# Optimization experiments

Measured on AMD Instinct MI355X. Metric: run time of the kernel, lower is better.

The kernel has to match this reference:

```python
import jax, jax.numpy as jnp
import numpy as np

N = 100000      # nodes
E = 1600000     # edges (avg degree 16)
F_IN = 256      # num_features
H2 = 128        # nhid * 2 (layer 1 width)
H = 64          # nhid (layer 2 width)
C = 10          # num_classes


def setup_inputs() -> dict:
    key = jax.random.key(0)
    ks = jax.random.split(key, 8)
    x = jax.random.normal(ks[0], (N, F_IN), dtype=jnp.float32)
    edge_index = jax.random.randint(ks[1], (2, E), 0, N, dtype=jnp.int64)
    W1 = jax.random.normal(ks[2], (F_IN, H2), dtype=jnp.float32) / np.float32(np.sqrt(F_IN))
    b1 = jnp.zeros((H2,), jnp.float32)
    W2 = jax.random.normal(ks[3], (H2, H), dtype=jnp.float32) / np.float32(np.sqrt(H2))
    b2 = jnp.zeros((H,), jnp.float32)
    Wl = jax.random.normal(ks[4], (H, C), dtype=jnp.float32) / np.float32(np.sqrt(H))
    bl = jnp.zeros((C,), jnp.float32)
    return {"x": x, "edge_index": edge_index, "W1": W1, "b1": b1,
            "W2": W2, "b2": b2, "Wl": Wl, "bl": bl}


def reference(x, edge_index, W1, b1, W2, b2, Wl, bl):
    # --- GCN normalization with self-loops (PyG GCNConv default) ---
    loops = jnp.arange(N, dtype=edge_index.dtype)
    src = jnp.concatenate([edge_index[0], loops])  # message sources
    dst = jnp.concatenate([edge_index[1], loops])  # message targets
    deg = jax.ops.segment_sum(jnp.ones(src.shape[0], x.dtype), dst, num_segments=N)
    dinv = jnp.where(deg > 0, jax.lax.rsqrt(deg), 0.0)
    norm = dinv[src] * dinv[dst]                   # [E+N]

    def gcn_conv(h, W, b):
        m = h @ W                                  # transform first (out_channels small)
        agg = jax.ops.segment_sum(m[src] * norm[:, None], dst, num_segments=N)
        return agg + b

    h = jax.nn.relu(gcn_conv(x, W1, b1))           # [N, H2]
    h = jax.nn.relu(gcn_conv(h, W2, b2))           # [N, H]
    logits = h @ Wl + bl                            # [N, C]
    return jax.nn.log_softmax(logits, axis=-1)
```

## Files before the change

kernel.cpp:

```cpp
#include <hip/hip_runtime.h>


typedef unsigned short ushort_t;
typedef unsigned int uint_t;
typedef __attribute__((ext_vector_type(8))) short short8;
typedef __attribute__((ext_vector_type(4))) float floatx4;

static __device__ __forceinline__ ushort_t f2bf(float f) {
    union { float f; uint_t u; } c; c.f = f;
    return (ushort_t)((c.u + 0x8000u) >> 16);
}
static __device__ __forceinline__ float bf2f(ushort_t h) {
    union { uint_t u; float f; } c; c.u = ((uint_t)h) << 16;
    return c.f;
}
static __device__ __forceinline__ float2 up2(uint_t p) {
    union { uint_t u; float f; } lo, hi;
    lo.u = p << 16; hi.u = p & 0xffff0000u;
    return make_float2(lo.f, hi.f);
}
static __device__ __forceinline__ uint_t pk2bf(float a, float b) {
    return ((uint_t)f2bf(b) << 16) | (uint_t)f2bf(a);
}
static __device__ __forceinline__ void ld_lds16(void* lds, const void* g) {
    __builtin_amdgcn_global_load_lds(
        (const __attribute__((address_space(1))) unsigned int*)g,
        (__attribute__((address_space(3))) unsigned int*)lds, 16, 0, 0);
}

#define NBMAX 800
#define ECAP  4096

__global__ __launch_bounds__(256) void hist_kernel(
    const int* __restrict__ dst, int* __restrict__ histG, int E, int NB) {
    __shared__ int h[NBMAX];
    for (int i = threadIdx.x; i < NB; i += 256) h[i] = 0;
    __syncthreads();
    int i8 = (blockIdx.x * 256 + threadIdx.x) * 8;
    if (i8 + 7 < E) {
        int4 d0 = *(const int4*)(dst + i8);
        int4 d1 = *(const int4*)(dst + i8 + 4);
        atomicAdd(&h[d0.x >> 7], 1);
        atomicAdd(&h[d0.y >> 7], 1);
        atomicAdd(&h[d0.z >> 7], 1);
        atomicAdd(&h[d0.w >> 7], 1);
        atomicAdd(&h[d1.x >> 7], 1);
        atomicAdd(&h[d1.y >> 7], 1);
        atomicAdd(&h[d1.z >> 7], 1);
        atomicAdd(&h[d1.w >> 7], 1);
    } else {
        for (int e = i8; e < E; e++) atomicAdd(&h[dst[e] >> 7], 1);
    }
    __syncthreads();
    int* out = histG + (size_t)blockIdx.x * NB;
    for (int i = threadIdx.x; i < NB; i += 256) out[i] = h[i];
}

__global__ __launch_bounds__(256) void scan_bucket(
    int* __restrict__ histG, int* __restrict__ totG, int GB, int NB) {
    __shared__ int s[256];
    const int b = blockIdx.x;
    const int t = threadIdx.x;
    int running = 0;
    int nch = (GB + 255) / 256;
    for (int c = 0; c < nch; c++) {
        int j = c * 256 + t;
        int v = (j < GB) ? histG[(size_t)j * NB + b] : 0;
        s[t] = v;
        __syncthreads();
        for (int off = 1; off < 256; off <<= 1) {
            int tmp = (t >= off) ? s[t - off] : 0;
            __syncthreads();
            s[t] += tmp;
            __syncthreads();
        }
        if (j < GB) histG[(size_t)j * NB + b] = s[t] - v + running;
        int ctot = s[255];
        __syncthreads();
        running += ctot;
    }
    if (t == 0) totG[b] = running;
}

__global__ void scan_tot(const int* __restrict__ totG, int* __restrict__ bbase,
                         int NB) {
    __shared__ int s[256];
    const int t = threadIdx.x;
    int running = 0;
    int nch = (NB + 255) / 256;
    for (int c = 0; c < nch; c++) {
        int j = c * 256 + t;
        int v = (j < NB) ? totG[j] : 0;
        s[t] = v;
        __syncthreads();
        for (int off = 1; off < 256; off <<= 1) {
            int tmp = (t >= off) ? s[t - off] : 0;
            __syncthreads();
            s[t] += tmp;
            __syncthreads();
        }
        if (j < NB) bbase[j] = s[t] - v + running;
        int ctot = s[255];
        __syncthreads();
        running += ctot;
    }
    if (t == 0) bbase[NB] = running;
}

__global__ __launch_bounds__(256) void scatter_kernel(
    const int* __restrict__ src, const int* __restrict__ dst,
    const int* __restrict__ histG, const int* __restrict__ bbase,
    int* __restrict__ packed, int E, int NB) {
    __shared__ int lbase[NBMAX];
    const int* row = histG + (size_t)blockIdx.x * NB;
    for (int i = threadIdx.x; i < NB; i += 256)
        lbase[i] = bbase[i] + row[i];
    __syncthreads();
    int i8 = (blockIdx.x * 256 + threadIdx.x) * 8;
    if (i8 + 7 < E) {
        int4 s0 = *(const int4*)(src + i8);
        int4 s1 = *(const int4*)(src + i8 + 4);
        int4 d0 = *(const int4*)(dst + i8);
        int4 d1 = *(const int4*)(dst + i8 + 4);
        int p;
        p = atomicAdd(&lbase[d0.x >> 7], 1); packed[p] = s0.x | ((d0.x & 127) << 17);
        p = atomicAdd(&lbase[d0.y >> 7], 1); packed[p] = s0.y | ((d0.y & 127) << 17);
        p = atomicAdd(&lbase[d0.z >> 7], 1); packed[p] = s0.z | ((d0.z & 127) << 17);
        p = atomicAdd(&lbase[d0.w >> 7], 1); packed[p] = s0.w | ((d0.w & 127) << 17);
        p = atomicAdd(&lbase[d1.x >> 7], 1); packed[p] = s1.x | ((d1.x & 127) << 17);
        p = atomicAdd(&lbase[d1.y >> 7], 1); packed[p] = s1.y | ((d1.y & 127) << 17);
        p = atomicAdd(&lbase[d1.z >> 7], 1); packed[p] = s1.z | ((d1.z & 127) << 17);
        p = atomicAdd(&lbase[d1.w >> 7], 1); packed[p] = s1.w | ((d1.w & 127) << 17);
    } else {
        for (int e = i8; e < E; e++) {
            int d = dst[e];
            int p = atomicAdd(&lbase[d >> 7], 1);
            packed[p] = src[e] | ((d & 127) << 17);
        }
    }
}

__global__ __launch_bounds__(256) void bucket_csr(
    const int* __restrict__ packed, const int* __restrict__ bbase,
    int* __restrict__ rowptr, int* __restrict__ csr,
    float* __restrict__ dinv, int N, int NB) {
    __shared__ int ebuf[ECAP];
    __shared__ int cnt[128];
    __shared__ int pl[128];
    __shared__ int s[256];
    const int b = blockIdx.x;
    const int t = threadIdx.x;
    const int lo = bbase[b];
    const int hi = bbase[b + 1];
    int m = hi - lo;
    if (m > ECAP) m = ECAP;
    for (int i = t; i < m; i += 256) ebuf[i] = packed[lo + i];
    if (t < 128) cnt[t] = 0;
    __syncthreads();
    for (int i = t; i < m; i += 256) atomicAdd(&cnt[ebuf[i] >> 17], 1);
    __syncthreads();
    const int node0 = b << 7;
    int c = (t < 128) ? cnt[t] : 0;
    if (t < 128 && node0 + t < N)
        dinv[node0 + t] = rsqrtf((float)(c + 1));
    s[t] = c;
    __syncthreads();
    for (int off = 1; off < 256; off <<= 1) {
        int tmp = (t >= off) ? s[t - off] : 0;
        __syncthreads();
        s[t] += tmp;
        __syncthreads();
    }
    int excl = s[t] - c;
    if (t < 128) {
        pl[t] = excl;
        if (node0 + t <= N) rowptr[node0 + t] = lo + excl;
    }
    __syncthreads();
    for (int i = t; i < m; i += 256) {
        int e = ebuf[i];
        int p = atomicAdd(&pl[e >> 17], 1);
        csr[lo + p] = e & 0x1FFFF;
    }
}

__global__ void wcvt2_kernel(const float* __restrict__ W1, const float* __restrict__ W2,
                             ushort_t* __restrict__ W1t, ushort_t* __restrict__ W2t) {
    int i = blockIdx.x * 256 + threadIdx.x;
    if (i < 256 * 128) {
        int k = i / 128, n = i % 128;
        W1t[n * 256 + k] = f2bf(W1[i]);
    }
    int j = i - 256 * 128;
    if (j >= 0 && j < 128 * 64) {
        int k = j / 64, n = j % 64;
        W2t[n * 128 + k] = f2bf(W2[j]);
    }
}

__global__ __launch_bounds__(256) void gemm1_mfma(
    const float* __restrict__ A, const ushort_t* __restrict__ Bt,
    const float* __restrict__ dinv, ushort_t* __restrict__ out, int M) {
    __shared__ ushort_t As[2][128 * 40];
    __shared__ ushort_t Bs[2][128 * 32];
    const int tid = threadIdx.x;
    const int l = tid & 63;
    const int wave = tid >> 6;
    const int wm = wave >> 1, wn = wave & 1;
    const int lrow = l & 15, hh = l >> 4;
    const int m0 = blockIdx.x * 128;

    const int srow = tid >> 1, sh = tid & 1;
    int grow = m0 + srow; if (grow >= M) grow = M - 1;
    const float* gA = A + (size_t)grow * 256 + sh * 16;
    const int wslot = srow * 40 + sh * 16;

    int aslot[4], bslot[4];
    #pragma unroll
    for (int mt = 0; mt < 4; mt++) {
        int r = wm * 64 + mt * 16 + lrow;
        aslot[mt] = r * 40 + hh * 8;
    }
    #pragma unroll
    for (int nt = 0; nt < 4; nt++) {
        int nc = wn * 64 + nt * 16 + lrow;
        bslot[nt] = (nc * 4 + (hh ^ ((nc >> 2) & 3))) * 8;
    }

    floatx4 acc[4][4];
    #pragma unroll
    for (int mt = 0; mt < 4; mt++)
        #pragma unroll
        for (int nt = 0; nt < 4; nt++)
            acc[mt][nt] = (floatx4){0.f, 0.f, 0.f, 0.f};

    float4 ar[4];
    auto loadA = [&](int k0) {
        #pragma unroll
        for (int i = 0; i < 4; i++)
            ar[i] = *(const float4*)(gA + k0 + i * 4);
    };
    auto writeA = [&](int buf) {
        uint4 q0, q1;
        q0.x = pk2bf(ar[0].x, ar[0].y); q0.y = pk2bf(ar[0].z, ar[0].w);
        q0.z = pk2bf(ar[1].x, ar[1].y); q0.w = pk2bf(ar[1].z, ar[1].w);
        q1.x = pk2bf(ar[2].x, ar[2].y); q1.y = pk2bf(ar[2].z, ar[2].w);
        q1.z = pk2bf(ar[3].x, ar[3].y); q1.w = pk2bf(ar[3].z, ar[3].w);
        *(uint4*)&As[buf][wslot] = q0;
        *(uint4*)&As[buf][wslot + 8] = q1;
    };
    auto stageB = [&](int buf, int k0) {
        #pragma unroll
        for (int i = 0; i < 2; i++) {
            int s = i * 256 + tid;
            int nn = s >> 2, cp = s & 3;
            int cg = cp ^ ((nn >> 2) & 3);
            ld_lds16(&Bs[buf][s * 8], Bt + (size_t)nn * 256 + k0 + cg * 8);
        }
    };

    loadA(0);
    stageB(0, 0);
    writeA(0);
    __syncthreads();

    int buf = 0;
    for (int kk = 0; kk < 8; kk++) {
        if (kk < 7) {
            loadA((kk + 1) * 32);
            stageB(buf ^ 1, (kk + 1) * 32);
        }
        short8 afr[4], bfr[4];
        #pragma unroll
        for (int mt = 0; mt < 4; mt++)
            afr[mt] = *(const short8*)&As[buf][aslot[mt]];
        #pragma unroll
        for (int nt = 0; nt < 4; nt++)
            bfr[nt] = *(const short8*)&Bs[buf][bslot[nt]];
        #pragma unroll
        for (int mt = 0; mt < 4; mt++)
            #pragma unroll
            for (int nt = 0; nt < 4; nt++)
                acc[mt][nt] = __builtin_amdgcn_mfma_f32_16x16x32_bf16(
                    afr[mt], bfr[nt], acc[mt][nt], 0, 0, 0);
        if (kk < 7) writeA(buf ^ 1);
        __syncthreads();
        buf ^= 1;
    }

    const int r0 = hh * 4;
    #pragma unroll
    for (int mt = 0; mt < 4; mt++) {
        int mbase = m0 + wm * 64 + mt * 16 + r0;
        float4 dv = *(const float4*)&dinv[mbase];
        float d[4] = {dv.x, dv.y, dv.z, dv.w};
        #pragma unroll
        for (int i = 0; i < 4; i++) {
            int m = mbase + i;
            if (m < M) {
                #pragma unroll
                for (int nt = 0; nt < 4; nt++)
                    out[(size_t)m * 128 + wn * 64 + nt * 16 + lrow] =
                        f2bf(acc[mt][nt][i] * d[i]);
            }
        }
    }
}

__global__ __launch_bounds__(256) void gemm2_mfma(
    const ushort_t* __restrict__ A, const ushort_t* __restrict__ Bt,
    const float* __restrict__ dinv, ushort_t* __restrict__ out, int M) {
    __shared__ ushort_t As[2][128 * 32];
    __shared__ ushort_t Bs[2][64 * 32];
    const int tid = threadIdx.x;
    const int l = tid & 63;
    const int wave = tid >> 6;
    const int wm = wave >> 1, wn = wave & 1;
    const int lrow = l & 15, hh = l >> 4;
    const int m0 = blockIdx.x * 128;

    int aslot[4], bslot[2];
    #pragma unroll
    for (int mt = 0; mt < 4; mt++) {
        int r = wm * 64 + mt * 16 + lrow;
        aslot[mt] = (r * 4 + (hh ^ ((r >> 2) & 3))) * 8;
    }
    #pragma unroll
    for (int nt = 0; nt < 2; nt++) {
        int nc = wn * 32 + nt * 16 + lrow;
        bslot[nt] = (nc * 4 + (hh ^ ((nc >> 2) & 3))) * 8;
    }

    floatx4 acc[4][2];
    #pragma unroll
    for (int mt = 0; mt < 4; mt++)
        #pragma unroll
        for (int nt = 0; nt < 2; nt++)
            acc[mt][nt] = (floatx4){0.f, 0.f, 0.f, 0.f};

    auto stage = [&](int buf, int k0) {
        #pragma unroll
        for (int i = 0; i < 2; i++) {
            int s = i * 256 + tid;
            int r = s >> 2, cp = s & 3;
            int cg = cp ^ ((r >> 2) & 3);
            int row = m0 + r; if (row >= M) row = M - 1;
            ld_lds16(&As[buf][s * 8], A + (size_t)row * 128 + k0 + cg * 8);
        }
        {
            int s = tid;
            int nn = s >> 2, cp = s & 3;
            int cg = cp ^ ((nn >> 2) & 3);
            ld_lds16(&Bs[buf][s * 8], Bt + (size_t)nn * 128 + k0 + cg * 8);
        }
    };

    stage(0, 0);
    __syncthreads();
    int buf = 0;
    for (int kk = 0; kk < 4; kk++) {
        if (kk < 3) stage(buf ^ 1, (kk + 1) * 32);
        short8 afr[4], bfr[2];
        #pragma unroll
        for (int mt = 0; mt < 4; mt++)
            afr[mt] = *(const short8*)&As[buf][aslot[mt]];
        #pragma unroll
        for (int nt = 0; nt < 2; nt++)
            bfr[nt] = *(const short8*)&Bs[buf][bslot[nt]];
        #pragma unroll
        for (int mt = 0; mt < 4; mt++)
            #pragma unroll
            for (int nt = 0; nt < 2; nt++)
                acc[mt][nt] = __builtin_amdgcn_mfma_f32_16x16x32_bf16(
                    afr[mt], bfr[nt], acc[mt][nt], 0, 0, 0);
        __syncthreads();
        buf ^= 1;
    }

    const int r0 = hh * 4;
    #pragma unroll
    for (int mt = 0; mt < 4; mt++) {
        int mbase = m0 + wm * 64 + mt * 16 + r0;
        float4 dv = *(const float4*)&dinv[mbase];
        float d[4] = {dv.x, dv.y, dv.z, dv.w};
        #pragma unroll
        for (int i = 0; i < 4; i++) {
            int m = mbase + i;
            if (m < M) {
                #pragma unroll
                for (int nt = 0; nt < 2; nt++)
                    out[(size_t)m * 64 + wn * 32 + nt * 16 + lrow] =
                        f2bf(acc[mt][nt][i] * d[i]);
            }
        }
    }
}

__global__ __launch_bounds__(256) void spmm_relu128(
    const ushort_t* __restrict__ Mm, const int* __restrict__ rowptr,
    const int* __restrict__ csr, const float* __restrict__ dinv,
    const float* __restrict__ bias, ushort_t* __restrict__ out, int n, int doff) {
    int v = (blockIdx.x * 256 + threadIdx.x) >> 6;
    int lane = threadIdx.x & 63;
    if (v >= n) return;
    int jb = rowptr[v];
    int cntn = rowptr[v + 1] - jb;
    const char* Mb = (const char*)Mm;
    const int slot = lane >> 4;
    const int q = lane & 15;
    const uint_t qb = (uint_t)q * 16;

    float2 a0 = {0.f, 0.f}, a1 = a0, a2 = a0, a3 = a0;
    if (slot == 0) {
        uint4 s = *(const uint4*)(Mb + ((size_t)v << 8) + qb);
        a0 = up2(s.x); a1 = up2(s.y); a2 = up2(s.z); a3 = up2(s.w);
    }

    for (int base = 0; base < cntn; base += 64) {
        int m = cntn - base; if (m > 64) m = 64;
        int roff = (base + lane < cntn) ? (csr[jb + base + lane] << 8) : doff;
        int m4 = (m + 3) & ~3;
        int jj = 0;
        for (; jj + 16 <= m4; jj += 16) {
            uint_t o[4];
            #pragma unroll
            for (int t = 0; t < 4; t++)
                o[t] = (uint_t)__shfl(roff, jj + 4 * t + slot) + qb;
            uint4 p[4];
            #pragma unroll
            for (int t = 0; t < 4; t++) p[t] = *(const uint4*)(Mb + o[t]);
            #pragma unroll
            for (int t = 0; t < 4; t++) {
                float2 f;
                f = up2(p[t].x); a0.x += f.x; a0.y += f.y;
                f = up2(p[t].y); a1.x += f.x; a1.y += f.y;
                f = up2(p[t].z); a2.x += f.x; a2.y += f.y;
                f = up2(p[t].w); a3.x += f.x; a3.y += f.y;
            }
        }
        for (; jj < m4; jj += 4) {
            uint_t o = (uint_t)__shfl(roff, jj + slot) + qb;
            uint4 p = *(const uint4*)(Mb + o);
            float2 f;
            f = up2(p.x); a0.x += f.x; a0.y += f.y;
            f = up2(p.y); a1.x += f.x; a1.y += f.y;
            f = up2(p.z); a2.x += f.x; a2.y += f.y;
            f = up2(p.w); a3.x += f.x; a3.y += f.y;
        }
    }
    float r[8] = {a0.x, a0.y, a1.x, a1.y, a2.x, a2.y, a3.x, a3.y};
    #pragma unroll
    for (int i = 0; i < 8; i++) r[i] += __shfl_xor(r[i], 16);
    #pragma unroll
    for (int i = 0; i < 8; i++) r[i] += __shfl_xor(r[i], 32);
    if (slot == 0) {
        float d = dinv[v];
        float4 bv0 = *(const float4*)&bias[q * 8];
        float4 bv1 = *(const float4*)&bias[q * 8 + 4];
        float o0 = fmaxf(d * r[0] + bv0.x, 0.f);
        float o1 = fmaxf(d * r[1] + bv0.y, 0.f);
        float o2 = fmaxf(d * r[2] + bv0.z, 0.f);
        float o3 = fmaxf(d * r[3] + bv0.w, 0.f);
        float o4 = fmaxf(d * r[4] + bv1.x, 0.f);
        float o5 = fmaxf(d * r[5] + bv1.y, 0.f);
        float o6 = fmaxf(d * r[6] + bv1.z, 0.f);
        float o7 = fmaxf(d * r[7] + bv1.w, 0.f);
        uint4 pk;
        pk.x = pk2bf(o0, o1); pk.y = pk2bf(o2, o3);
        pk.z = pk2bf(o4, o5); pk.w = pk2bf(o6, o7);
        *(uint4*)(out + (size_t)v * 128 + q * 8) = pk;
    }
}

__global__ __launch_bounds__(256) void spmm_relu64(
    const ushort_t* __restrict__ Mm, const int* __restrict__ rowptr,
    const int* __restrict__ csr, const float* __restrict__ dinv,
    const float* __restrict__ bias, ushort_t* __restrict__ out, int n, int doff) {
    int v = (blockIdx.x * 256 + threadIdx.x) >> 6;
    int lane = threadIdx.x & 63;
    if (v >= n) return;
    int jb = rowptr[v];
    int cntn = rowptr[v + 1] - jb;
    const char* Mb = (const char*)Mm;
    const int slot = lane >> 3;
    const int q = lane & 7;
    const uint_t qb = (uint_t)q * 16;

    float2 a0 = {0.f, 0.f}, a1 = a0, a2 = a0, a3 = a0;
    if (slot == 0) {
        uint4 s = *(const uint4*)(Mb + ((size_t)v << 7) + qb);
        a0 = up2(s.x); a1 = up2(s.y); a2 = up2(s.z); a3 = up2(s.w);
    }

    for (int base = 0; base < cntn; base += 64) {
        int m = cntn - base; if (m > 64) m = 64;
        int roff = (base + lane < cntn) ? (csr[jb + base + lane] << 7) : doff;
        int m8 = (m + 7) & ~7;
        int jj = 0;
        for (; jj + 16 <= m8; jj += 16) {
            uint_t o[2];
            #pragma unroll
            for (int t = 0; t < 2; t++)
                o[t] = (uint_t)__shfl(roff, jj + 8 * t + slot) + qb;
            uint4 p[2];
            #pragma unroll
            for (int t = 0; t < 2; t++) p[t] = *(const uint4*)(Mb + o[t]);
            #pragma unroll
            for (int t = 0; t < 2; t++) {
                float2 f;
                f = up2(p[t].x); a0.x += f.x; a0.y += f.y;
                f = up2(p[t].y); a1.x += f.x; a1.y += f.y;
                f = up2(p[t].z); a2.x += f.x; a2.y += f.y;
                f = up2(p[t].w); a3.x += f.x; a3.y += f.y;
            }
        }
        for (; jj < m8; jj += 8) {
            uint_t o = (uint_t)__shfl(roff, jj + slot) + qb;
            uint4 p = *(const uint4*)(Mb + o);
            float2 f;
            f = up2(p.x); a0.x += f.x; a0.y += f.y;
            f = up2(p.y); a1.x += f.x; a1.y += f.y;
            f = up2(p.z); a2.x += f.x; a2.y += f.y;
            f = up2(p.w); a3.x += f.x; a3.y += f.y;
        }
    }
    float r[8] = {a0.x, a0.y, a1.x, a1.y, a2.x, a2.y, a3.x, a3.y};
    #pragma unroll
    for (int i = 0; i < 8; i++) r[i] += __shfl_xor(r[i], 8);
    #pragma unroll
    for (int i = 0; i < 8; i++) r[i] += __shfl_xor(r[i], 16);
    #pragma unroll
    for (int i = 0; i < 8; i++) r[i] += __shfl_xor(r[i], 32);
    if (slot == 0) {
        float d = dinv[v];
        float4 bv0 = *(const float4*)&bias[q * 8];
        float4 bv1 = *(const float4*)&bias[q * 8 + 4];
        float o0 = fmaxf(d * r[0] + bv0.x, 0.f);
        float o1 = fmaxf(d * r[1] + bv0.y, 0.f);
        float o2 = fmaxf(d * r[2] + bv0.z, 0.f);
        float o3 = fmaxf(d * r[3] + bv0.w, 0.f);
        float o4 = fmaxf(d * r[4] + bv1.x, 0.f);
        float o5 = fmaxf(d * r[5] + bv1.y, 0.f);
        float o6 = fmaxf(d * r[6] + bv1.z, 0.f);
        float o7 = fmaxf(d * r[7] + bv1.w, 0.f);
        uint4 pk;
        pk.x = pk2bf(o0, o1); pk.y = pk2bf(o2, o3);
        pk.z = pk2bf(o4, o5); pk.w = pk2bf(o6, o7);
        *(uint4*)(out + (size_t)v * 64 + q * 8) = pk;
    }
}

__global__ __launch_bounds__(256) void head_kernel(
    const ushort_t* __restrict__ h2, const float* __restrict__ Wl,
    const float* __restrict__ bl, float* __restrict__ out, int n) {
    __shared__ float Ws[64 * 10];
    __shared__ float bs[10];
    for (int i = threadIdx.x; i < 640; i += 256) Ws[i] = Wl[i];
    if (threadIdx.x < 10) bs[threadIdx.x] = bl[threadIdx.x];
    __syncthreads();
    int v = blockIdx.x * 256 + threadIdx.x;
    if (v >= n) return;
    float acc[10];
    #pragma unroll
    for (int c = 0; c < 10; c++) acc[c] = bs[c];
    const ushort_t* hrow = &h2[(size_t)v * 64];
    #pragma unroll
    for (int k0 = 0; k0 < 64; k0 += 8) {
        short8 hv = *(const short8*)&hrow[k0];
        #pragma unroll
        for (int kk = 0; kk < 8; kk++) {
            float hf = bf2f((ushort_t)hv[kk]);
            #pragma unroll
            for (int c = 0; c < 10; c++)
                acc[c] += hf * Ws[(k0 + kk) * 10 + c];
        }
    }
    float m = acc[0];
    #pragma unroll
    for (int c = 1; c < 10; c++) m = fmaxf(m, acc[c]);
    float s = 0.f;
    #pragma unroll
    for (int c = 0; c < 10; c++) s += expf(acc[c] - m);
    float lse = logf(s);
    #pragma unroll
    for (int c = 0; c < 10; c++) out[(size_t)v * 10 + c] = acc[c] - m - lse;
}

extern "C" void kernel_launch(void* const* d_in, const int* in_sizes, int n_in,
                              void* d_out, int out_size, void* d_ws, size_t ws_size,
                              hipStream_t stream) {
    const float* x   = (const float*)d_in[0];
    const int*   ei  = (const int*)d_in[1];
    const float* W1  = (const float*)d_in[2];
    const float* b1  = (const float*)d_in[3];
    const float* W2  = (const float*)d_in[4];
    const float* b2  = (const float*)d_in[5];
    const float* Wl  = (const float*)d_in[6];
    const float* bl  = (const float*)d_in[7];
    float*       out = (float*)d_out;

    const int N = in_sizes[0] / 256;
    const int E = in_sizes[1] / 2;
    const int* srcI = ei;
    const int* dstI = ei + E;

    const int NB = (N + 127) >> 7;
    const int GB = (E + 2047) / 2048;

    char* ws = (char*)d_ws;
    size_t off = 0;
    auto alloc = [&](size_t bytes) -> void* {
        void* p = ws + off;
        off = (off + bytes + 255) & ~(size_t)255;
        return p;
    };
    int*      histG  = (int*)alloc((size_t)GB * NB * 4);
    int*      totG   = (int*)alloc((size_t)NB * 4);
    int*      bbase  = (int*)alloc((size_t)(NB + 1) * 4);
    int*      packed = (int*)alloc((size_t)E * 4);
    int*      rowptr = (int*)alloc((size_t)(N + 1) * 4);
    float*    dinv   = (float*)alloc((size_t)(N + 128) * 4);
    int*      csr    = (int*)alloc((size_t)E * 4);
    ushort_t* W1t    = (ushort_t*)alloc((size_t)128 * 256 * 2);
    ushort_t* W2t    = (ushort_t*)alloc((size_t)64 * 128 * 2);
    ushort_t* bufA   = (ushort_t*)alloc((size_t)(N + 2) * 128 * 2);
    ushort_t* bufB   = (ushort_t*)alloc((size_t)N * 128 * 2);

    hist_kernel<<<GB, 256, 0, stream>>>(dstI, histG, E, NB);
    scan_bucket<<<NB, 256, 0, stream>>>(histG, totG, GB, NB);
    scan_tot<<<1, 256, 0, stream>>>(totG, bbase, NB);
    scatter_kernel<<<GB, 256, 0, stream>>>(srcI, dstI, histG, bbase, packed, E, NB);
    bucket_csr<<<NB, 256, 0, stream>>>(packed, bbase, rowptr, csr, dinv, N, NB);

    wcvt2_kernel<<<(256 * 128 + 128 * 64 + 255) / 256, 256, 0, stream>>>(W1, W2, W1t, W2t);

    const int gblk = (N + 127) / 128;
    gemm1_mfma<<<gblk, 256, 0, stream>>>(x, W1t, dinv, bufA, N);
    hipMemsetAsync(bufA + (size_t)N * 128, 0, 256, stream);
    spmm_relu128<<<(N + 3) / 4, 256, 0, stream>>>(bufA, rowptr, csr, dinv, b1, bufB, N, N << 8);
    gemm2_mfma<<<gblk, 256, 0, stream>>>(bufB, W2t, dinv, bufA, N);
    hipMemsetAsync(bufA + (size_t)N * 64, 0, 128, stream);
    spmm_relu64<<<(N + 3) / 4, 256, 0, stream>>>(bufA, rowptr, csr, dinv, b2, bufB, N, N << 7);
    head_kernel<<<(N + 255) / 256, 256, 0, stream>>>(bufB, Wl, bl, out, N);
}
```

Before: 362.7 us.

## Drop LDS staging in GEMMs, serialize per-bucket scan, double edges per thread

Both MFMA GEMMs now load A and B fragments straight from global memory into registers, with no LDS double-buffering. Each wave owns 32 rows and the full output width, so the block barriers go away but B is re-read by every wave. The bucket scan becomes one thread per bucket doing a sequential column scan over a halved number of histogram rows. Histogram and scatter kernels now process 16 edges per thread, which halves the histogram size and the scan work. Possible costs are uncoalesced column access in the scan, less overlap in the GEMMs, and more LDS atomic contention per block.

Result: slower. 374.3 us (+3.2%).

```diff
diff --git a/kernel.cpp b/kernel.cpp
--- a/kernel.cpp
+++ b/kernel.cpp
@@ -22,11 +22,6 @@
 static __device__ __forceinline__ uint_t pk2bf(float a, float b) {
     return ((uint_t)f2bf(b) << 16) | (uint_t)f2bf(a);
 }
-static __device__ __forceinline__ void ld_lds16(void* lds, const void* g) {
-    __builtin_amdgcn_global_load_lds(
-        (const __attribute__((address_space(1))) unsigned int*)g,
-        (__attribute__((address_space(3))) unsigned int*)lds, 16, 0, 0);
-}
 
 #define NBMAX 800
 #define ECAP  4096
@@ -36,20 +31,18 @@
     __shared__ int h[NBMAX];
     for (int i = threadIdx.x; i < NB; i += 256) h[i] = 0;
     __syncthreads();
-    int i8 = (blockIdx.x * 256 + threadIdx.x) * 8;
-    if (i8 + 7 < E) {
-        int4 d0 = *(const int4*)(dst + i8);
-        int4 d1 = *(const int4*)(dst + i8 + 4);
-        atomicAdd(&h[d0.x >> 7], 1);
-        atomicAdd(&h[d0.y >> 7], 1);
-        atomicAdd(&h[d0.z >> 7], 1);
-        atomicAdd(&h[d0.w >> 7], 1);
-        atomicAdd(&h[d1.x >> 7], 1);
-        atomicAdd(&h[d1.y >> 7], 1);
-        atomicAdd(&h[d1.z >> 7], 1);
-        atomicAdd(&h[d1.w >> 7], 1);
+    int i16 = (blockIdx.x * 256 + threadIdx.x) * 16;
+    if (i16 + 15 < E) {
+        #pragma unroll
+        for (int u = 0; u < 4; u++) {
+            int4 d = *(const int4*)(dst + i16 + u * 4);
+            atomicAdd(&h[d.x >> 7], 1);
+            atomicAdd(&h[d.y >> 7], 1);
+            atomicAdd(&h[d.z >> 7], 1);
+            atomicAdd(&h[d.w >> 7], 1);
+        }
     } else {
-        for (int e = i8; e < E; e++) atomicAdd(&h[dst[e] >> 7], 1);
+        for (int e = i16; e < E; e++) atomicAdd(&h[dst[e] >> 7], 1);
     }
     __syncthreads();
     int* out = histG + (size_t)blockIdx.x * NB;
@@ -58,28 +51,26 @@
 
 __global__ __launch_bounds__(256) void scan_bucket(
     int* __restrict__ histG, int* __restrict__ totG, int GB, int NB) {
-    __shared__ int s[256];
-    const int b = blockIdx.x;
-    const int t = threadIdx.x;
-    int running = 0;
-    int nch = (GB + 255) / 256;
-    for (int c = 0; c < nch; c++) {
-        int j = c * 256 + t;
-        int v = (j < GB) ? histG[(size_t)j * NB + b] : 0;
-        s[t] = v;
-        __syncthreads();
-        for (int off = 1; off < 256; off <<= 1) {
-            int tmp = (t >= off) ? s[t - off] : 0;
-            __syncthreads();
-            s[t] += tmp;
-            __syncthreads();
-        }
-        if (j < GB) histG[(size_t)j * NB + b] = s[t] - v + running;
-        int ctot = s[255];
-        __syncthreads();
-        running += ctot;
-    }
-    if (t == 0) totG[b] = running;
+    int b = blockIdx.x * 256 + threadIdx.x;
+    if (b >= NB) return;
+    int run = 0;
+    int g = 0;
+    for (; g + 16 <= GB; g += 16) {
+        int vv[16];
+        #pragma unroll
+        for (int u = 0; u < 16; u++) vv[u] = histG[(size_t)(g + u) * NB + b];
+        #pragma unroll
+        for (int u = 0; u < 16; u++) {
+            histG[(size_t)(g + u) * NB + b] = run;
+            run += vv[u];
+        }
+    }
+    for (; g < GB; g++) {
+        int v = histG[(size_t)g * NB + b];
+        histG[(size_t)g * NB + b] = run;
+        run += v;
+    }
+    totG[b] = run;
 }
 
 __global__ void scan_tot(const int* __restrict__ totG, int* __restrict__ bbase,
@@ -116,23 +107,20 @@
     for (int i = threadIdx.x; i < NB; i += 256)
         lbase[i] = bbase[i] + row[i];
     __syncthreads();
-    int i8 = (blockIdx.x * 256 + threadIdx.x) * 8;
-    if (i8 + 7 < E) {
-        int4 s0 = *(const int4*)(src + i8);
-        int4 s1 = *(const int4*)(src + i8 + 4);
-        int4 d0 = *(const int4*)(dst + i8);
-        int4 d1 = *(const int4*)(dst + i8 + 4);
-        int p;
-        p = atomicAdd(&lbase[d0.x >> 7], 1); packed[p] = s0.x | ((d0.x & 127) << 17);
-        p = atomicAdd(&lbase[d0.y >> 7], 1); packed[p] = s0.y | ((d0.y & 127) << 17);
-        p = atomicAdd(&lbase[d0.z >> 7], 1); packed[p] = s0.z | ((d0.z & 127) << 17);
-        p = atomicAdd(&lbase[d0.w >> 7], 1); packed[p] = s0.w | ((d0.w & 127) << 17);
-        p = atomicAdd(&lbase[d1.x >> 7], 1); packed[p] = s1.x | ((d1.x & 127) << 17);
-        p = atomicAdd(&lbase[d1.y >> 7], 1); packed[p] = s1.y | ((d1.y & 127) << 17);
-        p = atomicAdd(&lbase[d1.z >> 7], 1); packed[p] = s1.z | ((d1.z & 127) << 17);
-        p = atomicAdd(&lbase[d1.w >> 7], 1); packed[p] = s1.w | ((d1.w & 127) << 17);
+    int i16 = (blockIdx.x * 256 + threadIdx.x) * 16;
+    if (i16 + 15 < E) {
+        #pragma unroll
+        for (int u = 0; u < 4; u++) {
+            int4 s4 = *(const int4*)(src + i16 + u * 4);
+            int4 d4 = *(const int4*)(dst + i16 + u * 4);
+            int p;
+            p = atomicAdd(&lbase[d4.x >> 7], 1); packed[p] = s4.x | ((d4.x & 127) << 17);
+            p = atomicAdd(&lbase[d4.y >> 7], 1); packed[p] = s4.y | ((d4.y & 127) << 17);
+            p = atomicAdd(&lbase[d4.z >> 7], 1); packed[p] = s4.z | ((d4.z & 127) << 17);
+            p = atomicAdd(&lbase[d4.w >> 7], 1); packed[p] = s4.w | ((d4.w & 127) << 17);
+        }
     } else {
-        for (int e = i8; e < E; e++) {
+        for (int e = i16; e < E; e++) {
             int d = dst[e];
             int p = atomicAdd(&lbase[d >> 7], 1);
             packed[p] = src[e] | ((d & 127) << 17);
@@ -201,97 +189,130 @@
 __global__ __launch_bounds__(256) void gemm1_mfma(
     const float* __restrict__ A, const ushort_t* __restrict__ Bt,
     const float* __restrict__ dinv, ushort_t* __restrict__ out, int M) {
-    __shared__ ushort_t As[2][128 * 40];
-    __shared__ ushort_t Bs[2][128 * 32];
     const int tid = threadIdx.x;
     const int l = tid & 63;
     const int wave = tid >> 6;
-    const int wm = wave >> 1, wn = wave & 1;
     const int lrow = l & 15, hh = l >> 4;
-    const int m0 = blockIdx.x * 128;
-
-    const int srow = tid >> 1, sh = tid & 1;
-    int grow = m0 + srow; if (grow >= M) grow = M - 1;
-    const float* gA = A + (size_t)grow * 256 + sh * 16;
-    const int wslot = srow * 40 + sh * 16;
-
-    int aslot[4], bslot[4];
-    #pragma unroll
-    for (int mt = 0; mt < 4; mt++) {
-        int r = wm * 64 + mt * 16 + lrow;
-        aslot[mt] = r * 40 + hh * 8;
-    }
-    #pragma unroll
-    for (int nt = 0; nt < 4; nt++) {
-        int nc = wn * 64 + nt * 16 + lrow;
-        bslot[nt] = (nc * 4 + (hh ^ ((nc >> 2) & 3))) * 8;
-    }
-
-    floatx4 acc[4][4];
-    #pragma unroll
-    for (int mt = 0; mt < 4; mt++)
+    const int m0 = blockIdx.x * 128 + wave * 32;
+
+    const float* ga0;
+    const float* ga1;
+    {
+        int r0 = m0 + lrow;      if (r0 >= M) r0 = M - 1;
+        int r1 = m0 + 16 + lrow; if (r1 >= M) r1 = M - 1;
+        ga0 = A + (size_t)r0 * 256 + hh * 8;
+        ga1 = A + (size_t)r1 * 256 + hh * 8;
+    }
+    const ushort_t* gb = Bt + (size_t)lrow * 256 + hh * 8;
+
+    floatx4 acc[2][8];
+    #pragma unroll
+    for (int mt = 0; mt < 2; mt++)
+        #pragma unroll
+        for (int nt = 0; nt < 8; nt++)
+            acc[mt][nt] = (floatx4){0.f, 0.f, 0.f, 0.f};
+
+    for (int kk = 0; kk < 8; kk++) {
+        const int k0 = kk * 32;
+        short8 afr[2];
+        {
+            float4 u = *(const float4*)(ga0 + k0);
+            float4 v = *(const float4*)(ga0 + k0 + 4);
+            short8 t;
+            t[0] = (short)f2bf(u.x); t[1] = (short)f2bf(u.y);
+            t[2] = (short)f2bf(u.z); t[3] = (short)f2bf(u.w);
+            t[4] = (short)f2bf(v.x); t[5] = (short)f2bf(v.y);
+            t[6] = (short)f2bf(v.z); t[7] = (short)f2bf(v.w);
+            afr[0] = t;
+        }
+        {
+            float4 u = *(const float4*)(ga1 + k0);
+            float4 v = *(const float4*)(ga1 + k0 + 4);
+            short8 t;
+            t[0] = (short)f2bf(u.x); t[1] = (short)f2bf(u.y);
+            t[2] = (short)f2bf(u.z); t[3] = (short)f2bf(u.w);
+            t[4] = (short)f2bf(v.x); t[5] = (short)f2bf(v.y);
+            t[6] = (short)f2bf(v.z); t[7] = (short)f2bf(v.w);
+            afr[1] = t;
+        }
+        short8 bfr[8];
+        #pragma unroll
+        for (int nt = 0; nt < 8; nt++)
+            bfr[nt] = *(const short8*)(gb + (size_t)nt * 16 * 256 + k0);
+        #pragma unroll
+        for (int mt = 0; mt < 2; mt++)
+            #pragma unroll
+            for (int nt = 0; nt < 8; nt++)
+                acc[mt][nt] = __builtin_amdgcn_mfma_f32_16x16x32_bf16(
+                    afr[mt], bfr[nt], acc[mt][nt], 0, 0, 0);
+    }
+
+    const int r0 = hh * 4;
+    #pragma unroll
+    for (int mt = 0; mt < 2; mt++) {
+        int mbase = m0 + mt * 16 + r0;
+        float4 dv = *(const float4*)&dinv[mbase];
+        float d[4] = {dv.x, dv.y, dv.z, dv.w};
+        #pragma unroll
+        for (int i = 0; i < 4; i++) {
+            int m = mbase + i;
+            if (m < M) {
+                #pragma unroll
+                for (int nt = 0; nt < 8; nt++)
+                    out[(size_t)m * 128 + nt * 16 + lrow] =
+                        f2bf(acc[mt][nt][i] * d[i]);
+            }
+        }
+    }
+}
+
+__global__ __launch_bounds__(256) void gemm2_mfma(
+    const ushort_t* __restrict__ A, const ushort_t* __restrict__ Bt,
+    const float* __restrict__ dinv, ushort_t* __restrict__ out, int M) {
+    const int tid = threadIdx.x;
+    const int l = tid & 63;
+    const int wave = tid >> 6;
+    const int lrow = l & 15, hh = l >> 4;
+    const int m0 = blockIdx.x * 128 + wave * 32;
+
+    const ushort_t* ga0;
+    const ushort_t* ga1;
+    {
+        int r0 = m0 + lrow;      if (r0 >= M) r0 = M - 1;
+        int r1 = m0 + 16 + lrow; if (r1 >= M) r1 = M - 1;
+        ga0 = A + (size_t)r0 * 128 + hh * 8;
+        ga1 = A + (size_t)r1 * 128 + hh * 8;
+    }
+    const ushort_t* gb = Bt + (size_t)lrow * 128 + hh * 8;
+
+    floatx4 acc[2][4];
+    #pragma unroll
+    for (int mt = 0; mt < 2; mt++)
         #pragma unroll
         for (int nt = 0; nt < 4; nt++)
             acc[mt][nt] = (floatx4){0.f, 0.f, 0.f, 0.f};
 
-    float4 ar[4];
-    auto loadA = [&](int k0) {
-        #pragma unroll
-        for (int i = 0; i < 4; i++)
-            ar[i] = *(const float4*)(gA + k0 + i * 4);
-    };
-    auto writeA = [&](int buf) {
-        uint4 q0, q1;
-        q0.x = pk2bf(ar[0].x, ar[0].y); q0.y = pk2bf(ar[0].z, ar[0].w);
-        q0.z = pk2bf(ar[1].x, ar[1].y); q0.w = pk2bf(ar[1].z, ar[1].w);
-        q1.x = pk2bf(ar[2].x, ar[2].y); q1.y = pk2bf(ar[2].z, ar[2].w);
-        q1.z = pk2bf(ar[3].x, ar[3].y); q1.w = pk2bf(ar[3].z, ar[3].w);
-        *(uint4*)&As[buf][wslot] = q0;
-        *(uint4*)&As[buf][wslot + 8] = q1;
-    };
-    auto stageB = [&](int buf, int k0) {
-        #pragma unroll
-        for (int i = 0; i < 2; i++) {
-            int s = i * 256 + tid;
-            int nn = s >> 2, cp = s & 3;
-            int cg = cp ^ ((nn >> 2) & 3);
-            ld_lds16(&Bs[buf][s * 8], Bt + (size_t)nn * 256 + k0 + cg * 8);
-        }
-    };
-
-    loadA(0);
-    stageB(0, 0);
-    writeA(0);
-    __syncthreads();
-
-    int buf = 0;
-    for (int kk = 0; kk < 8; kk++) {
-        if (kk < 7) {
-            loadA((kk + 1) * 32);
-            stageB(buf ^ 1, (kk + 1) * 32);
-        }
-        short8 afr[4], bfr[4];
-        #pragma unroll
-        for (int mt = 0; mt < 4; mt++)
-            afr[mt] = *(const short8*)&As[buf][aslot[mt]];
+    for (int kk = 0; kk < 4; kk++) {
+        const int k0 = kk * 32;
+        short8 afr[2];
+        afr[0] = *(const short8*)(ga0 + k0);
+        afr[1] = *(const short8*)(ga1 + k0);
+        short8 bfr[4];
         #pragma unroll
         for (int nt = 0; nt < 4; nt++)
-            bfr[nt] = *(const short8*)&Bs[buf][bslot[nt]];
-        #pragma unroll
-        for (int mt = 0; mt < 4; mt++)
+            bfr[nt] = *(const short8*)(gb + (size_t)nt * 16 * 128 + k0);
+        #pragma unroll
+        for (int mt = 0; mt < 2; mt++)
             #pragma unroll
             for (int nt = 0; nt < 4; nt++)
                 acc[mt][nt] = __builtin_amdgcn_mfma_f32_16x16x32_bf16(
                     afr[mt], bfr[nt], acc[mt][nt], 0, 0, 0);
-        if (kk < 7) writeA(buf ^ 1);
-        __syncthreads();
-        buf ^= 1;
     }
 
     const int r0 = hh * 4;
     #pragma unroll
-    for (int mt = 0; mt < 4; mt++) {
-        int mbase = m0 + wm * 64 + mt * 16 + r0;
+    for (int mt = 0; mt < 2; mt++) {
+        int mbase = m0 + mt * 16 + r0;
         float4 dv = *(const float4*)&dinv[mbase];
         float d[4] = {dv.x, dv.y, dv.z, dv.w};
         #pragma unroll
@@ -300,96 +321,7 @@
             if (m < M) {
                 #pragma unroll
                 for (int nt = 0; nt < 4; nt++)
-                    out[(size_t)m * 128 + wn * 64 + nt * 16 + lrow] =
-                        f2bf(acc[mt][nt][i] * d[i]);
-            }
-        }
-    }
-}
-
-__global__ __launch_bounds__(256) void gemm2_mfma(
-    const ushort_t* __restrict__ A, const ushort_t* __restrict__ Bt,
-    const float* __restrict__ dinv, ushort_t* __restrict__ out, int M) {
-    __shared__ ushort_t As[2][128 * 32];
-    __shared__ ushort_t Bs[2][64 * 32];
-    const int tid = threadIdx.x;
-    const int l = tid & 63;
-    const int wave = tid >> 6;
-    const int wm = wave >> 1, wn = wave & 1;
-    const int lrow = l & 15, hh = l >> 4;
-    const int m0 = blockIdx.x * 128;
-
-    int aslot[4], bslot[2];
-    #pragma unroll
-    for (int mt = 0; mt < 4; mt++) {
-        int r = wm * 64 + mt * 16 + lrow;
-        aslot[mt] = (r * 4 + (hh ^ ((r >> 2) & 3))) * 8;
-    }
-    #pragma unroll
-    for (int nt = 0; nt < 2; nt++) {
-        int nc = wn * 32 + nt * 16 + lrow;
-        bslot[nt] = (nc * 4 + (hh ^ ((nc >> 2) & 3))) * 8;
-    }
-
-    floatx4 acc[4][2];
-    #pragma unroll
-    for (int mt = 0; mt < 4; mt++)
-        #pragma unroll
-        for (int nt = 0; nt < 2; nt++)
-            acc[mt][nt] = (floatx4){0.f, 0.f, 0.f, 0.f};
-
-    auto stage = [&](int buf, int k0) {
-        #pragma unroll
-        for (int i = 0; i < 2; i++) {
-            int s = i * 256 + tid;
-            int r = s >> 2, cp = s & 3;
-            int cg = cp ^ ((r >> 2) & 3);
-            int row = m0 + r; if (row >= M) row = M - 1;
-            ld_lds16(&As[buf][s * 8], A + (size_t)row * 128 + k0 + cg * 8);
-        }
-        {
-            int s = tid;
-            int nn = s >> 2, cp = s & 3;
-            int cg = cp ^ ((nn >> 2) & 3);
-            ld_lds16(&Bs[buf][s * 8], Bt + (size_t)nn * 128 + k0 + cg * 8);
-        }
-    };
-
-    stage(0, 0);
-    __syncthreads();
-    int buf = 0;
-    for (int kk = 0; kk < 4; kk++) {
-        if (kk < 3) stage(buf ^ 1, (kk + 1) * 32);
-        short8 afr[4], bfr[2];
-        #pragma unroll
-        for (int mt = 0; mt < 4; mt++)
-            afr[mt] = *(const short8*)&As[buf][aslot[mt]];
-        #pragma unroll
-        for (int nt = 0; nt < 2; nt++)
-            bfr[nt] = *(const short8*)&Bs[buf][bslot[nt]];
-        #pragma unroll
-        for (int mt = 0; mt < 4; mt++)
-            #pragma unroll
-            for (int nt = 0; nt < 2; nt++)
-                acc[mt][nt] = __builtin_amdgcn_mfma_f32_16x16x32_bf16(
-                    afr[mt], bfr[nt], acc[mt][nt], 0, 0, 0);
-        __syncthreads();
-        buf ^= 1;
-    }
-
-    const int r0 = hh * 4;
-    #pragma unroll
-    for (int mt = 0; mt < 4; mt++) {
-        int mbase = m0 + wm * 64 + mt * 16 + r0;
-        float4 dv = *(const float4*)&dinv[mbase];
-        float d[4] = {dv.x, dv.y, dv.z, dv.w};
-        #pragma unroll
-        for (int i = 0; i < 4; i++) {
-            int m = mbase + i;
-            if (m < M) {
-                #pragma unroll
-                for (int nt = 0; nt < 2; nt++)
-                    out[(size_t)m * 64 + wn * 32 + nt * 16 + lrow] =
+                    out[(size_t)m * 64 + nt * 16 + lrow] =
                         f2bf(acc[mt][nt][i] * d[i]);
             }
         }
@@ -605,7 +537,7 @@
     const int* dstI = ei + E;
 
     const int NB = (N + 127) >> 7;
-    const int GB = (E + 2047) / 2048;
+    const int GB = (E + 4095) / 4096;
 
     char* ws = (char*)d_ws;
     size_t off = 0;
@@ -627,7 +559,7 @@
     ushort_t* bufB   = (ushort_t*)alloc((size_t)N * 128 * 2);
 
     hist_kernel<<<GB, 256, 0, stream>>>(dstI, histG, E, NB);
-    scan_bucket<<<NB, 256, 0, stream>>>(histG, totG, GB, NB);
+    scan_bucket<<<(NB + 255) / 256, 256, 0, stream>>>(histG, totG, GB, NB);
     scan_tot<<<1, 256, 0, stream>>>(totG, bbase, NB);
     scatter_kernel<<<GB, 256, 0, stream>>>(srcI, dstI, histG, bbase, packed, E, NB);
     bucket_csr<<<NB, 256, 0, stream>>>(packed, bbase, rowptr, csr, dinv, N, NB);
```
